# Performance work log

Hardware: AMD Instinct MI355X
Metric: run time of the kernel (lower is better)

## Reference

```python
import jax, jax.numpy as jnp
import numpy as np

B, Q, H = 1, 1024, 2048
NH, NKV, HD = 32, 8, 64
KB = 2048
THETA = 10000.0
KB_MAX_TRAIN = 4096.0


def _bitlinear(x, w):
    """BitNet b1.58 linear: per-token int8 absmax activation quant + ternary weight quant (STE)."""
    a_scale = 127.0 / jnp.clip(jnp.max(jnp.abs(x), axis=-1, keepdims=True), 1e-5)
    xq = jnp.clip(jnp.round(x * a_scale), -128.0, 127.0) / a_scale
    w_scale = 1.0 / jnp.clip(jnp.mean(jnp.abs(w)), 1e-5)
    wq = jnp.clip(jnp.round(w * w_scale), -1.0, 1.0) / w_scale
    x_ste = x + jax.lax.stop_gradient(xq - x)
    w_ste = w + jax.lax.stop_gradient(wq - w)
    return jnp.einsum('bsh,oh->bso', x_ste, w_ste)


def _rope_cos_sin(position_ids):
    inv_freq = 1.0 / (THETA ** (jnp.arange(0, HD, 2, dtype=jnp.float32) / HD))  # [HD/2]
    freqs = position_ids.astype(jnp.float32)[..., None] * inv_freq  # [B,Q,HD/2]
    emb = jnp.concatenate([freqs, freqs], axis=-1)  # [B,Q,HD]
    return jnp.cos(emb)[:, None], jnp.sin(emb)[:, None]  # [B,1,Q,HD]


def _rotate_half(x):
    return jnp.concatenate([-x[..., HD // 2:], x[..., :HD // 2]], axis=-1)


def setup_inputs() -> dict:
    key = jax.random.key(0)
    ks = jax.random.split(key, 9)
    hidden_states = jax.random.normal(ks[0], (B, Q, H), jnp.float32)
    # additive causal mask
    attention_mask = jnp.triu(jnp.full((Q, Q), -1e9, jnp.float32), 1)[None, None]
    kb_keys = jax.random.normal(ks[1], (B, NH, KB, HD), jnp.float32)
    kb_values = jax.random.normal(ks[2], (B, NH, KB, HD), jnp.float32)
    s = 0.02
    Wq = jax.random.normal(ks[3], (NH * HD, H), jnp.float32) * s
    Wk = jax.random.normal(ks[4], (NKV * HD, H), jnp.float32) * s
    Wv = jax.random.normal(ks[5], (NKV * HD, H), jnp.float32) * s
    Wo = jax.random.normal(ks[6], (H, NH * HD), jnp.float32) * s
    Wq_new = jax.random.normal(ks[7], (NH * HD, H), jnp.float32) * s
    position_ids = jnp.arange(Q, dtype=jnp.int32)[None, :]
    return dict(hidden_states=hidden_states, attention_mask=attention_mask,
                kb_keys=kb_keys, kb_values=kb_values,
                Wq=Wq, Wk=Wk, Wv=Wv, Wo=Wo, Wq_new=Wq_new,
                position_ids=position_ids)


def reference(hidden_states, attention_mask, kb_keys, kb_values,
              Wq, Wk, Wv, Wo, Wq_new, position_ids):
    b, q_len, _ = hidden_states.shape
    # BitLinear QKV projections
    q = _bitlinear(hidden_states, Wq).reshape(b, q_len, NH, HD).transpose(0, 2, 1, 3)
    k = _bitlinear(hidden_states, Wk).reshape(b, q_len, NKV, HD).transpose(0, 2, 1, 3)
    v = _bitlinear(hidden_states, Wv).reshape(b, q_len, NKV, HD).transpose(0, 2, 1, 3)
    # RoPE on prompt q/k (KB query is NOT rotated, matching the source)
    cos, sin = _rope_cos_sin(position_ids)
    q = q * cos + _rotate_half(q) * sin
    k = k * cos + _rotate_half(k) * sin
    # GQA: repeat kv heads
    groups = NH // NKV
    k = jnp.repeat(k, groups, axis=1)
    v = jnp.repeat(v, groups, axis=1)
    # KB query via separate BitLinear
    kb_q = _bitlinear(hidden_states, Wq_new).reshape(b, q_len, NH, HD).transpose(0, 2, 1, 3)
    scale = 1.0 / jnp.sqrt(jnp.float32(HD))
    kb_len = kb_keys.shape[2]
    scores_kb = jnp.einsum('bhqd,bhkd->bhqk', kb_q, kb_keys) * scale
    scores_kb = scores_kb + (jnp.log(jnp.float32(KB_MAX_TRAIN)) - jnp.log(jnp.float32(kb_len)))
    scores_p = jnp.einsum('bhqd,bhkd->bhqk', q, k) * scale + attention_mask
    attn = jax.nn.softmax(jnp.concatenate([scores_kb, scores_p], axis=-1).astype(jnp.float32), axis=-1)
    out = (jnp.einsum('bhqk,bhkd->bhqd', attn[..., :kb_len], kb_values)
           + jnp.einsum('bhqk,bhkd->bhqd', attn[..., kb_len:], v))
    out = out.transpose(0, 2, 1, 3).reshape(b, q_len, NH * HD)
    return _bitlinear(out, Wo)
```

## Files before the change

### kernel.cpp

```cpp
#include <hip/hip_runtime.h>
#include <hip/hip_bf16.h>
#include <stdint.h>
#include <math.h>

#define cH    2048
#define cQ    1024
#define cNH   32
#define cNKV  8
#define cKB   2048

#define INV_BIG   (1.0f/4194304.0f)
#define INV_SMALL (1.0f/1048576.0f)

#define WS_SUMS 0
#define WS_DQ1  256
#define WS_DQ2  4352
#define WS_XQ   8448
#define WS_WALL 4202752
#define WS_QB   25174272
#define WS_KB   33562880
#define WS_VB   35660032
#define WS_QN   37757184
#define WS_ROPET 46145792


using short8  = __attribute__((ext_vector_type(8))) short;
using floatx4 = __attribute__((ext_vector_type(4))) float;

__device__ __forceinline__ void bsplit(float x, unsigned short& hi, unsigned short& lo) {
  __hip_bfloat16 h = __float2bfloat16(x);
  float hf = __bfloat162float(h);
  __hip_bfloat16 l = __float2bfloat16(x - hf);
  hi = *(unsigned short*)&h;
  lo = *(unsigned short*)&l;
}

__device__ __forceinline__ unsigned short tern(float v, float ws) {
  float q = rintf(v * ws);
  q = fminf(fmaxf(q, -1.0f), 1.0f);
  return (unsigned short)(__float_as_uint(q) >> 16);
}

__global__ void k_ropetab(const int* __restrict__ pos, float2* __restrict__ tab) {
  int i = blockIdx.x * 256 + threadIdx.x;
  int t = i >> 5, d = i & 31;
  double p = (double)pos[t];
  double ang = p * pow(10000.0, -(double)d / 32.0);
  tab[i] = make_float2((float)cos(ang), (float)sin(ang));
}

__global__ void k_abssum5(const float* __restrict__ w0, const float* __restrict__ w1,
                          const float* __restrict__ w2, const float* __restrict__ w3,
                          const float* __restrict__ w4, double* __restrict__ out) {
  __shared__ double red[256];
  const int seg = blockIdx.y;
  const float* w = seg == 0 ? w0 : seg == 1 ? w1 : seg == 2 ? w2 : seg == 3 ? w3 : w4;
  const int n4 = ((seg == 1 || seg == 2) ? 512 * 2048 : 2048 * 2048) / 4;
  double s = 0.0;
  for (int i = blockIdx.x * 256 + threadIdx.x; i < n4; i += gridDim.x * 256) {
    float4 x = *(const float4*)(w + (size_t)i * 4);
    s += (double)fabsf(x.x) + (double)fabsf(x.y) + (double)fabsf(x.z) + (double)fabsf(x.w);
  }
  red[threadIdx.x] = s;
  __syncthreads();
  for (int o = 128; o > 0; o >>= 1) {
    if ((int)threadIdx.x < o) red[threadIdx.x] += red[threadIdx.x + o];
    __syncthreads();
  }
  if (threadIdx.x == 0) atomicAdd(out + seg, red[0]);
}

__global__ void k_wquant4(const float* __restrict__ Wq, const float* __restrict__ Wk,
                          const float* __restrict__ Wv, const float* __restrict__ Wqn,
                          unsigned short* __restrict__ wall, const double* __restrict__ sums) {
  size_t i = ((size_t)blockIdx.x * 256 + threadIdx.x) * 4;
  const float* src; size_t off; double s; float inv;
  if (i < 4194304)      { src = Wq;  off = 0;       s = sums[0]; inv = INV_BIG; }
  else if (i < 5242880) { src = Wk;  off = 4194304; s = sums[1]; inv = INV_SMALL; }
  else if (i < 6291456) { src = Wv;  off = 5242880; s = sums[2]; inv = INV_SMALL; }
  else                  { src = Wqn; off = 6291456; s = sums[4]; inv = INV_BIG; }
  float ws = 1.0f / fmaxf((float)s * inv, 1e-5f);
  float4 x = *(const float4*)(src + (i - off));
  ushort4 o;
  o.x = tern(x.x, ws); o.y = tern(x.y, ws); o.z = tern(x.z, ws); o.w = tern(x.w, ws);
  *(ushort4*)(wall + i) = o;
}

__global__ void k_wquant(const float* __restrict__ w, unsigned short* __restrict__ wq,
                         const double* __restrict__ sum, float inv_n) {
  size_t i = ((size_t)blockIdx.x * 256 + threadIdx.x) * 4;
  float ws = 1.0f / fmaxf((float)(*sum) * inv_n, 1e-5f);
  float4 x = *(const float4*)(w + i);
  ushort4 o;
  o.x = tern(x.x, ws); o.y = tern(x.y, ws); o.z = tern(x.z, ws); o.w = tern(x.w, ws);
  *(ushort4*)(wq + i) = o;
}

__global__ void k_aquant(const float* __restrict__ x, unsigned short* __restrict__ xq,
                         float* __restrict__ dq, int K) {
  int t = blockIdx.x;
  const float4* xr = (const float4*)(x + (size_t)t * K);
  const int K4 = K / 4;
  __shared__ float red[256];
  float m = 0.0f;
  for (int i = threadIdx.x; i < K4; i += 256) {
    float4 v = xr[i];
    m = fmaxf(m, fmaxf(fmaxf(fabsf(v.x), fabsf(v.y)), fmaxf(fabsf(v.z), fabsf(v.w))));
  }
  red[threadIdx.x] = m;
  __syncthreads();
  for (int o = 128; o > 0; o >>= 1) {
    if ((int)threadIdx.x < o) red[threadIdx.x] = fmaxf(red[threadIdx.x], red[threadIdx.x + o]);
    __syncthreads();
  }
  float amax = fmaxf(red[0], 1e-5f);
  float as = 127.0f / amax;
  ushort4* xo = (ushort4*)(xq + (size_t)t * K);
  for (int i = threadIdx.x; i < K4; i += 256) {
    float4 v = xr[i];
    ushort4 o;
    float q;
    q = fminf(fmaxf(rintf(v.x * as), -128.0f), 127.0f); o.x = (unsigned short)(__float_as_uint(q) >> 16);
    q = fminf(fmaxf(rintf(v.y * as), -128.0f), 127.0f); o.y = (unsigned short)(__float_as_uint(q) >> 16);
    q = fminf(fmaxf(rintf(v.z * as), -128.0f), 127.0f); o.z = (unsigned short)(__float_as_uint(q) >> 16);
    q = fminf(fmaxf(rintf(v.w * as), -128.0f), 127.0f); o.w = (unsigned short)(__float_as_uint(q) >> 16);
    xo[i] = o;
  }
  if (threadIdx.x == 0) dq[t] = amax / 127.0f;
}

__global__ __launch_bounds__(256) void k_gemm_mfma(
    const unsigned short* __restrict__ Aq, const unsigned short* __restrict__ Ball,
    const float* __restrict__ adq, const double* __restrict__ sums,
    const float2* __restrict__ ropetab,
    float* __restrict__ oQ, unsigned short* __restrict__ oKhi,
    unsigned short* __restrict__ oKlo,
    float* __restrict__ oV, float* __restrict__ oQN, int mode) {
  __shared__ unsigned short As[128 * 72];
  __shared__ unsigned short Bs[128 * 72];
  const int t = threadIdx.x;
  const int lane = t & 63;
  const int row16 = lane & 15, q = lane >> 4;
  const int w = t >> 6;
  const int wm = (w >> 1) * 64, wn = (w & 1) * 64;
  const int bx = blockIdx.x;
  const int m0 = blockIdx.y * 128;
  const unsigned short* Bp = Ball + (size_t)bx * 128 * 2048;

  floatx4 acc[4][4];
#pragma unroll
  for (int g = 0; g < 4; ++g)
#pragma unroll
    for (int h = 0; h < 4; ++h) acc[g][h] = (floatx4){0.f, 0.f, 0.f, 0.f};

  for (int k0 = 0; k0 < 2048; k0 += 64) {
#pragma unroll
    for (int i = 0; i < 4; ++i) {
      int c = t + 256 * i;
      int row = c >> 3, g8 = c & 7;
      *(uint4*)&As[row * 72 + g8 * 8] =
          *(const uint4*)(Aq + (size_t)(m0 + row) * 2048 + k0 + g8 * 8);
      *(uint4*)&Bs[row * 72 + g8 * 8] =
          *(const uint4*)(Bp + (size_t)row * 2048 + k0 + g8 * 8);
    }
    __syncthreads();
#pragma unroll
    for (int kk = 0; kk < 2; ++kk) {
      short8 af[4], bf[4];
#pragma unroll
      for (int g = 0; g < 4; ++g)
        af[g] = *(const short8*)&As[(wm + g * 16 + row16) * 72 + kk * 32 + q * 8];
#pragma unroll
      for (int h = 0; h < 4; ++h)
        bf[h] = *(const short8*)&Bs[(wn + h * 16 + row16) * 72 + kk * 32 + q * 8];
#pragma unroll
      for (int g = 0; g < 4; ++g)
#pragma unroll
        for (int h = 0; h < 4; ++h)
          acc[g][h] = __builtin_amdgcn_mfma_f32_16x16x32_bf16(af[g], bf[h], acc[g][h], 0, 0, 0);
    }
    __syncthreads();
  }

  float* outp = nullptr; int Nout = 0, nb0; float wdq;
  if (mode == 1)      { outp = oQ;  Nout = 2048; nb0 = bx * 128;        wdq = fmaxf((float)sums[3] * INV_BIG,   1e-5f); }
  else if (bx < 16)   { outp = oQ;  Nout = 2048; nb0 = bx * 128;        wdq = fmaxf((float)sums[0] * INV_BIG,   1e-5f); }
  else if (bx < 20)   {             Nout = 512;  nb0 = (bx - 16) * 128; wdq = fmaxf((float)sums[1] * INV_SMALL, 1e-5f); }
  else if (bx < 24)   { outp = oV;  Nout = 512;  nb0 = (bx - 20) * 128; wdq = fmaxf((float)sums[2] * INV_SMALL, 1e-5f); }
  else                { outp = oQN; Nout = 2048; nb0 = (bx - 24) * 128; wdq = fmaxf((float)sums[4] * INV_BIG,   1e-5f); }

  if (mode == 0 && bx < 20) {
#pragma unroll
    for (int g = 0; g < 4; ++g)
#pragma unroll
      for (int r = 0; r < 4; ++r) {
        int m = m0 + wm + g * 16 + q * 4 + r;
        float s = adq[m] * wdq;
        float2 cs0 = ropetab[m * 32 + row16];
        float2 cs1 = ropetab[m * 32 + 16 + row16];
        float v0 = acc[g][0][r] * s, v1 = acc[g][1][r] * s;
        float v2 = acc[g][2][r] * s, v3 = acc[g][3][r] * s;
        float o0 = v0 * cs0.x - v2 * cs0.y;
        float o2 = v2 * cs0.x + v0 * cs0.y;
        float o1 = v1 * cs1.x - v3 * cs1.y;
        float o3 = v3 * cs1.x + v1 * cs1.y;
        if (bx < 16) {
          size_t base = (size_t)m * Nout + nb0 + wn;
          outp[base + row16]      = o0;
          outp[base + 16 + row16] = o1;
          outp[base + 32 + row16] = o2;
          outp[base + 48 + row16] = o3;
        } else {
          int hkv_ = (nb0 + wn) >> 6;
          int kt_ = m >> 6, rr = m & 63;
          size_t tb = ((size_t)(hkv_ * 16 + kt_)) * 4096;
          int lbase = (rr & 15) + ((row16 >> 3) << 4);
          int ntb = (rr >> 4) * 512 + (row16 & 7);
          unsigned short hi, lo; int ix;
          bsplit(o0, hi, lo); ix = ntb + (lbase     ) * 8;          oKhi[tb + ix] = hi; oKlo[tb + ix] = lo;
          bsplit(o1, hi, lo); ix = ntb + (lbase + 32) * 8;          oKhi[tb + ix] = hi; oKlo[tb + ix] = lo;
          bsplit(o2, hi, lo); ix = ntb + (lbase     ) * 8 + 2048;   oKhi[tb + ix] = hi; oKlo[tb + ix] = lo;
          bsplit(o3, hi, lo); ix = ntb + (lbase + 32) * 8 + 2048;   oKhi[tb + ix] = hi; oKlo[tb + ix] = lo;
        }
      }
  } else {
#pragma unroll
    for (int g = 0; g < 4; ++g)
#pragma unroll
      for (int r = 0; r < 4; ++r) {
        int m = m0 + wm + g * 16 + q * 4 + r;
        float s = adq[m] * wdq;
#pragma unroll
        for (int h = 0; h < 4; ++h)
          outp[(size_t)m * Nout + nb0 + wn + h * 16 + row16] = acc[g][h][r] * s;
      }
  }
}

__global__ __launch_bounds__(256) void k_prep(
    const float* __restrict__ kbv, const float* __restrict__ Vb,
    unsigned short* __restrict__ vtKBhi, unsigned short* __restrict__ vtPhi,
    float* __restrict__ kbk) {
  const int b = blockIdx.x;
  const int t = threadIdx.x;
  if (b >= 1152) {
    float* tile = kbk + (size_t)(b - 1152) * 4096;
    float v[2][8];
#pragma unroll
    for (int u = 0; u < 2; ++u) {
      int task = t + 256 * u;
      int r = task >> 3, s = task & 7;
      *(float4*)&v[u][0] = *(const float4*)(tile + r * 64 + s * 8);
      *(float4*)&v[u][4] = *(const float4*)(tile + r * 64 + s * 8 + 4);
    }
    __syncthreads();
    unsigned short* up = (unsigned short*)tile;
#pragma unroll
    for (int u = 0; u < 2; ++u) {
      int task = t + 256 * u;
      int r = task >> 3, s = task & 7;
      union { unsigned short u16[8]; uint4 q; } hi, lo;
#pragma unroll
      for (int j = 0; j < 8; ++j) bsplit(v[u][j], hi.u16[j], lo.u16[j]);
      size_t off = (size_t)(((s >> 2) * 4 + (r >> 4)) * 512 + ((r & 15) + ((s & 3) << 4)) * 8);
      *(uint4*)(up + off)        = hi.q;
      *(uint4*)(up + 4096 + off) = lo.q;
    }
    return;
  }
  __shared__ float Lf[64 * 65];
  const float* src; unsigned short *dhi, *dlo; int srcStride;
  if (b < 1024) {
    int h = b >> 5, kt = b & 31;
    src = kbv + ((size_t)h * cKB + kt * 64) * 64; srcStride = 64;
    dhi = vtKBhi + (size_t)b * 4096; dlo = dhi + 4194304;
  } else {
    int bb = b - 1024;
    int hkv = bb >> 4, kt = bb & 15;
    src = Vb + (size_t)(kt * 64) * 512 + hkv * 64; srcStride = 512;
    dhi = vtPhi + (size_t)bb * 4096; dlo = dhi + 524288;
  }
#pragma unroll
  for (int i = 0; i < 4; ++i) {
    int c = t + 256 * i;
    int row = c >> 4, c4 = (c & 15) * 4;
    float4 x = *(const float4*)(src + (size_t)row * srcStride + c4);
    Lf[row * 65 + c4 + 0] = x.x;
    Lf[row * 65 + c4 + 1] = x.y;
    Lf[row * 65 + c4 + 2] = x.z;
    Lf[row * 65 + c4 + 3] = x.w;
  }
  __syncthreads();
#pragma unroll
  for (int u = 0; u < 2; ++u) {
    int task = t + 256 * u;
    int d = task >> 3, s = task & 7;
    union { unsigned short u16[8]; uint4 q; } hi, lo;
#pragma unroll
    for (int j = 0; j < 8; ++j) bsplit(Lf[(s * 8 + j) * 65 + d], hi.u16[j], lo.u16[j]);
    size_t off = (size_t)(((s >> 2) * 4 + (d >> 4)) * 512 + ((d & 15) + ((s & 3) << 4)) * 8);
    *(uint4*)(dhi + off) = hi.q;
    *(uint4*)(dlo + off) = lo.q;
  }
}

__global__ __launch_bounds__(256, 2) void k_attn_mfma(
    const float* __restrict__ Qr, float* qnctx,
    const unsigned short* __restrict__ KPhi,
    const unsigned short* __restrict__ kbkS,
    const unsigned short* __restrict__ vtKBhi,
    const unsigned short* __restrict__ vtPhi) {
  __shared__ __attribute__((aligned(16))) unsigned int Pbuf[4][16 * 68];

  const int t = threadIdx.x;
  const int lane = t & 63;
  const int col = lane & 15;
  const int quad = lane >> 4;
  const int w = t >> 6;
  const int h = blockIdx.x;
  const int q0 = blockIdx.y * 64;
  const int hkv = h >> 2;
  const float kbbias = 0.69314718055994531f;
  unsigned int* Pw = &Pbuf[w][0];
  const int fl = lane * 8;

  short8 qAh[2], qAl[2];
  short8 qBh[2], qBl[2];
  {
#pragma unroll
    for (int kk = 0; kk < 2; ++kk) {
      const size_t off = (size_t)(q0 + w * 16 + col) * 2048 + h * 64 + kk * 32 + quad * 8;
      float4 a = *(const float4*)(qnctx + off);
      float4 b = *(const float4*)(qnctx + off + 4);
      float xs[8] = {a.x, a.y, a.z, a.w, b.x, b.y, b.z, b.w};
#pragma unroll
      for (int j = 0; j < 8; ++j) {
        unsigned short hi, lo;
        bsplit(xs[j] * 0.125f, hi, lo);
        qAh[kk][j] = (short)hi; qAl[kk][j] = (short)lo;
      }
      float4 c = *(const float4*)(Qr + off);
      float4 d = *(const float4*)(Qr + off + 4);
      float ys[8] = {c.x, c.y, c.z, c.w, d.x, d.y, d.z, d.w};
#pragma unroll
      for (int j = 0; j < 8; ++j) {
        unsigned short hi, lo;
        bsplit(ys[j] * 0.125f, hi, lo);
        qBh[kk][j] = (short)hi; qBl[kk][j] = (short)lo;
      }
    }
  }

  floatx4 acco[4];
  float m_[4], l_[4];
#pragma unroll
  for (int nt = 0; nt < 4; ++nt) acco[nt] = (floatx4){0.f, 0.f, 0.f, 0.f};
#pragma unroll
  for (int r = 0; r < 4; ++r) { m_[r] = -3.0e38f; l_[r] = 0.f; }

  const int ntiles = 32 + (q0 >> 6) + 1;

  short8 kh[2][4], kl[2][4];
  short8 vh[2][4], vl[2][4];

  auto loadK = [&](int kt2) {
    const unsigned short *ph, *pl;
    if (kt2 < 32) { const size_t tk = (size_t)(h * 32 + kt2);
                    ph = kbkS + tk * 8192; pl = ph + 4096; }
    else          { const size_t tk = (size_t)(hkv * 16 + (kt2 - 32));
                    ph = KPhi + tk * 4096; pl = ph + 524288; }
#pragma unroll
    for (int kk = 0; kk < 2; ++kk)
#pragma unroll
      for (int nt = 0; nt < 4; ++nt) {
        kh[kk][nt] = *(const short8*)(ph + (kk * 4 + nt) * 512 + fl);
        kl[kk][nt] = *(const short8*)(pl + (kk * 4 + nt) * 512 + fl);
      }
  };
  auto loadV = [&](int kt2) {
    const unsigned short *ph, *pl;
    if (kt2 < 32) { const size_t tk = (size_t)(h * 32 + kt2);
                    ph = vtKBhi + tk * 4096; pl = ph + 4194304; }
    else          { const size_t tk = (size_t)(hkv * 16 + (kt2 - 32));
                    ph = vtPhi + tk * 4096; pl = ph + 524288; }
#pragma unroll
    for (int kk = 0; kk < 2; ++kk)
#pragma unroll
      for (int nt = 0; nt < 4; ++nt) {
        vh[kk][nt] = *(const short8*)(ph + (kk * 4 + nt) * 512 + fl);
        vl[kk][nt] = *(const short8*)(pl + (kk * 4 + nt) * 512 + fl);
      }
  };

  loadK(0);

  for (int kt = 0; kt < ntiles; ++kt) {
    const bool isKB = kt < 32;
    loadV(kt);
    __builtin_amdgcn_s_barrier();

    floatx4 accs[4];
#pragma unroll
    for (int nt = 0; nt < 4; ++nt) accs[nt] = (floatx4){0.f, 0.f, 0.f, 0.f};
    if (isKB) {
#pragma unroll
      for (int kk = 0; kk < 2; ++kk)
#pragma unroll
        for (int nt = 0; nt < 4; ++nt) {
          accs[nt] = __builtin_amdgcn_mfma_f32_16x16x32_bf16(qAh[kk], kh[kk][nt], accs[nt], 0, 0, 0);
          accs[nt] = __builtin_amdgcn_mfma_f32_16x16x32_bf16(qAl[kk], kh[kk][nt], accs[nt], 0, 0, 0);
          accs[nt] = __builtin_amdgcn_mfma_f32_16x16x32_bf16(qAh[kk], kl[kk][nt], accs[nt], 0, 0, 0);
        }
    } else {
#pragma unroll
      for (int kk = 0; kk < 2; ++kk)
#pragma unroll
        for (int nt = 0; nt < 4; ++nt) {
          accs[nt] = __builtin_amdgcn_mfma_f32_16x16x32_bf16(qBh[kk], kh[kk][nt], accs[nt], 0, 0, 0);
          accs[nt] = __builtin_amdgcn_mfma_f32_16x16x32_bf16(qBl[kk], kh[kk][nt], accs[nt], 0, 0, 0);
          accs[nt] = __builtin_amdgcn_mfma_f32_16x16x32_bf16(qBh[kk], kl[kk][nt], accs[nt], 0, 0, 0);
        }
    }

    float sv[4][4];
    if (isKB) {
#pragma unroll
      for (int nt = 0; nt < 4; ++nt)
#pragma unroll
        for (int r = 0; r < 4; ++r) sv[nt][r] = accs[nt][r] + kbbias;
    } else if (kt < ntiles - 1) {
#pragma unroll
      for (int nt = 0; nt < 4; ++nt)
#pragma unroll
        for (int r = 0; r < 4; ++r) sv[nt][r] = accs[nt][r];
    } else {
#pragma unroll
      for (int nt = 0; nt < 4; ++nt) {
        int kl_ = nt * 16 + col;
#pragma unroll
        for (int r = 0; r < 4; ++r) {
          int ql_ = w * 16 + quad * 4 + r;
          sv[nt][r] = accs[nt][r] + ((kl_ <= ql_) ? 0.0f : -1e9f);
        }
      }
    }
#pragma unroll
    for (int r = 0; r < 4; ++r) {
      float rmax = fmaxf(fmaxf(sv[0][r], sv[1][r]), fmaxf(sv[2][r], sv[3][r]));
#pragma unroll
      for (int off = 8; off; off >>= 1) rmax = fmaxf(rmax, __shfl_xor(rmax, off));
      float mnew = fmaxf(m_[r], rmax);
      float alpha = __expf(m_[r] - mnew);
      float psum = 0.f;
#pragma unroll
      for (int nt = 0; nt < 4; ++nt) {
        float p = __expf(sv[nt][r] - mnew);
        sv[nt][r] = p;
        psum += p;
      }
#pragma unroll
      for (int off = 8; off; off >>= 1) psum += __shfl_xor(psum, off);
      l_[r] = l_[r] * alpha + psum;
      m_[r] = mnew;
#pragma unroll
      for (int nt = 0; nt < 4; ++nt) acco[nt][r] *= alpha;
    }

    loadK(kt + 1 < ntiles ? kt + 1 : kt);

#pragma unroll
    for (int nt = 0; nt < 4; ++nt)
#pragma unroll
      for (int r = 0; r < 4; ++r) {
        unsigned xb = __float_as_uint(sv[nt][r]);
        float hf = __uint_as_float(xb & 0xffff0000u);
        unsigned db = __float_as_uint(sv[nt][r] - hf);
        Pw[(quad * 4 + r) * 68 + nt * 16 + col] = (xb >> 16) | (db & 0xffff0000u);
      }

#pragma unroll
    for (int kk = 0; kk < 2; ++kk) {
      uint4 pa = *(const uint4*)&Pw[col * 68 + kk * 32 + quad * 8];
      uint4 pb = *(const uint4*)&Pw[col * 68 + kk * 32 + quad * 8 + 4];
      union { unsigned int u[4]; short8 s; } uh, ul;
      uh.u[0] = (pa.x & 0xffffu) | (pa.y << 16);
      uh.u[1] = (pa.z & 0xffffu) | (pa.w << 16);
      uh.u[2] = (pb.x & 0xffffu) | (pb.y << 16);
      uh.u[3] = (pb.z & 0xffffu) | (pb.w << 16);
      ul.u[0] = (pa.x >> 16) | (pa.y & 0xffff0000u);
      ul.u[1] = (pa.z >> 16) | (pa.w & 0xffff0000u);
      ul.u[2] = (pb.x >> 16) | (pb.y & 0xffff0000u);
      ul.u[3] = (pb.z >> 16) | (pb.w & 0xffff0000u);
      short8 ph8 = uh.s, pl8 = ul.s;
#pragma unroll
      for (int nt = 0; nt < 4; ++nt) {
        acco[nt] = __builtin_amdgcn_mfma_f32_16x16x32_bf16(ph8, vh[kk][nt], acco[nt], 0, 0, 0);
        acco[nt] = __builtin_amdgcn_mfma_f32_16x16x32_bf16(pl8, vh[kk][nt], acco[nt], 0, 0, 0);
        acco[nt] = __builtin_amdgcn_mfma_f32_16x16x32_bf16(ph8, vl[kk][nt], acco[nt], 0, 0, 0);
      }
    }
  }

#pragma unroll
  for (int r = 0; r < 4; ++r) {
    float linv = 1.0f / l_[r];
#pragma unroll
    for (int nt = 0; nt < 4; ++nt)
      qnctx[(size_t)(q0 + w * 16 + quad * 4 + r) * 2048 + h * 64 + nt * 16 + col] =
          acco[nt][r] * linv;
  }
}

extern "C" void kernel_launch(void* const* d_in, const int* in_sizes, int n_in,
                              void* d_out, int out_size, void* d_ws, size_t ws_size,
                              hipStream_t stream) {
  (void)in_sizes; (void)n_in; (void)out_size; (void)ws_size;
  const float* hidden = (const float*)d_in[0];
  float* kbk = (float*)d_in[2];
  const float* kbv = (const float*)d_in[3];
  const float* Wq  = (const float*)d_in[4];
  const float* Wk  = (const float*)d_in[5];
  const float* Wv  = (const float*)d_in[6];
  const float* Wo  = (const float*)d_in[7];
  const float* Wqn = (const float*)d_in[8];
  const int*   pos = (const int*)d_in[9];

  char* ws = (char*)d_ws;
  double* sums = (double*)(ws + WS_SUMS);
  float* dq1 = (float*)(ws + WS_DQ1);
  float* dq2 = (float*)(ws + WS_DQ2);
  unsigned short* xq   = (unsigned short*)(ws + WS_XQ);
  unsigned short* wall = (unsigned short*)(ws + WS_WALL);
  unsigned short* vtKBhi = (unsigned short*)(ws + WS_WALL);
  unsigned short* vtPhi  = (unsigned short*)(ws + WS_WALL + 16777216);
  unsigned short* wqo  = (unsigned short*)(ws + WS_QB);
  float* Qb  = (float*)(ws + WS_QB);
  unsigned short* KPhi = (unsigned short*)(ws + WS_KB);
  unsigned short* KPlo = KPhi + 524288;
  float* Vb  = (float*)(ws + WS_VB);
  float* QNC = (float*)(ws + WS_QN);
  float2* ropetab = (float2*)(ws + WS_ROPET);

  hipMemsetAsync(sums, 0, 64, stream);

  k_ropetab<<<128, 256, 0, stream>>>(pos, ropetab);
  k_abssum5<<<dim3(128, 5), 256, 0, stream>>>(Wq, Wk, Wv, Wo, Wqn, sums);
  k_wquant4<<<10240, 256, 0, stream>>>(Wq, Wk, Wv, Wqn, wall, sums);
  k_aquant<<<cQ, 256, 0, stream>>>(hidden, xq, dq1, cH);

  k_gemm_mfma<<<dim3(40, 8), 256, 0, stream>>>(xq, wall, dq1, sums, ropetab,
                                               Qb, KPhi, KPlo, Vb, QNC, 0);

  k_prep<<<1152 + 1024, 256, 0, stream>>>(kbv, Vb, vtKBhi, vtPhi, kbk);

  k_attn_mfma<<<dim3(cNH, cQ / 64), 256, 0, stream>>>(
      Qb, QNC, KPhi, (const unsigned short*)kbk, vtKBhi, vtPhi);

  k_wquant<<<4096, 256, 0, stream>>>(Wo, wqo, sums + 3, INV_BIG);
  k_aquant<<<cQ, 256, 0, stream>>>(QNC, xq, dq2, cH);

  k_gemm_mfma<<<dim3(16, 8), 256, 0, stream>>>(xq, wqo, dq2, sums, ropetab,
                                               (float*)d_out, nullptr, nullptr,
                                               nullptr, nullptr, 1);
}
```

Before: 392.0 us.

## Split attention into KB and prompt passes with a separate softmax merge

The attention kernel now launches a second grid dimension so the knowledge-base keys and the causal prompt keys run in separate blocks. Each block writes an unnormalized partial output and its running max and sum, and a new merge kernel combines the two partials with rescaled softmax weights. This doubles the block count, shortens the serial tile loop per block, removes per-tile branching and halves the Q registers held, with launch bounds raised to allow more occupancy. In exchange it costs an extra kernel launch plus an extra round trip of partial outputs through global memory.

```diff
diff --git a/kernel.cpp b/kernel.cpp
--- a/kernel.cpp
+++ b/kernel.cpp
@@ -22,6 +22,7 @@
 #define WS_VB   35660032
 #define WS_QN   37757184
 #define WS_ROPET 46145792
+#define WS_ML   46407936
 
 
 using short8  = __attribute__((ext_vector_type(8))) short;
@@ -304,12 +305,13 @@
   }
 }
 
-__global__ __launch_bounds__(256, 2) void k_attn_mfma(
-    const float* __restrict__ Qr, float* qnctx,
+__global__ __launch_bounds__(256, 4) void k_attn_mfma(
+    float* __restrict__ Qr, float* __restrict__ qnctx,
     const unsigned short* __restrict__ KPhi,
     const unsigned short* __restrict__ kbkS,
     const unsigned short* __restrict__ vtKBhi,
-    const unsigned short* __restrict__ vtPhi) {
+    const unsigned short* __restrict__ vtPhi,
+    float2* __restrict__ ml) {
   __shared__ __attribute__((aligned(16))) unsigned int Pbuf[4][16 * 68];
 
   const int t = threadIdx.x;
@@ -319,34 +321,38 @@
   const int w = t >> 6;
   const int h = blockIdx.x;
   const int q0 = blockIdx.y * 64;
+  const int split = blockIdx.z;
   const int hkv = h >> 2;
   const float kbbias = 0.69314718055994531f;
   unsigned int* Pw = &Pbuf[w][0];
   const int fl = lane * 8;
 
-  short8 qAh[2], qAl[2];
-  short8 qBh[2], qBl[2];
+  const unsigned short *Kb, *Vbp; int Kstr, Kloo, Vloo, ntiles;
+  float* obase;
+  if (split == 0) {
+    Kb = kbkS + (size_t)h * 32 * 8192;   Kstr = 8192; Kloo = 4096;
+    Vbp = vtKBhi + (size_t)h * 32 * 4096; Vloo = 4194304;
+    ntiles = 32; obase = qnctx;
+  } else {
+    Kb = KPhi + (size_t)hkv * 16 * 4096; Kstr = 4096; Kloo = 524288;
+    Vbp = vtPhi + (size_t)hkv * 16 * 4096; Vloo = 524288;
+    ntiles = (q0 >> 6) + 1; obase = Qr;
+  }
+
+  short8 qh[2], ql[2];
   {
+    const float* qbase = split == 0 ? qnctx : Qr;
 #pragma unroll
     for (int kk = 0; kk < 2; ++kk) {
       const size_t off = (size_t)(q0 + w * 16 + col) * 2048 + h * 64 + kk * 32 + quad * 8;
-      float4 a = *(const float4*)(qnctx + off);
-      float4 b = *(const float4*)(qnctx + off + 4);
+      float4 a = *(const float4*)(qbase + off);
+      float4 b = *(const float4*)(qbase + off + 4);
       float xs[8] = {a.x, a.y, a.z, a.w, b.x, b.y, b.z, b.w};
 #pragma unroll
       for (int j = 0; j < 8; ++j) {
         unsigned short hi, lo;
         bsplit(xs[j] * 0.125f, hi, lo);
-        qAh[kk][j] = (short)hi; qAl[kk][j] = (short)lo;
-      }
-      float4 c = *(const float4*)(Qr + off);
-      float4 d = *(const float4*)(Qr + off + 4);
-      float ys[8] = {c.x, c.y, c.z, c.w, d.x, d.y, d.z, d.w};
-#pragma unroll
-      for (int j = 0; j < 8; ++j) {
-        unsigned short hi, lo;
-        bsplit(ys[j] * 0.125f, hi, lo);
-        qBh[kk][j] = (short)hi; qBl[kk][j] = (short)lo;
+        qh[kk][j] = (short)hi; ql[kk][j] = (short)lo;
       }
     }
   }
@@ -358,17 +364,12 @@
 #pragma unroll
   for (int r = 0; r < 4; ++r) { m_[r] = -3.0e38f; l_[r] = 0.f; }
 
-  const int ntiles = 32 + (q0 >> 6) + 1;
-
   short8 kh[2][4], kl[2][4];
   short8 vh[2][4], vl[2][4];
 
   auto loadK = [&](int kt2) {
-    const unsigned short *ph, *pl;
-    if (kt2 < 32) { const size_t tk = (size_t)(h * 32 + kt2);
-                    ph = kbkS + tk * 8192; pl = ph + 4096; }
-    else          { const size_t tk = (size_t)(hkv * 16 + (kt2 - 32));
-                    ph = KPhi + tk * 4096; pl = ph + 524288; }
+    const unsigned short* ph = Kb + (size_t)kt2 * Kstr;
+    const unsigned short* pl = ph + Kloo;
 #pragma unroll
     for (int kk = 0; kk < 2; ++kk)
 #pragma unroll
@@ -378,11 +379,8 @@
       }
   };
   auto loadV = [&](int kt2) {
-    const unsigned short *ph, *pl;
-    if (kt2 < 32) { const size_t tk = (size_t)(h * 32 + kt2);
-                    ph = vtKBhi + tk * 4096; pl = ph + 4194304; }
-    else          { const size_t tk = (size_t)(hkv * 16 + (kt2 - 32));
-                    ph = vtPhi + tk * 4096; pl = ph + 524288; }
+    const unsigned short* ph = Vbp + (size_t)kt2 * 4096;
+    const unsigned short* pl = ph + Vloo;
 #pragma unroll
     for (int kk = 0; kk < 2; ++kk)
 #pragma unroll
@@ -395,35 +393,23 @@
   loadK(0);
 
   for (int kt = 0; kt < ntiles; ++kt) {
-    const bool isKB = kt < 32;
     loadV(kt);
     __builtin_amdgcn_s_barrier();
 
     floatx4 accs[4];
 #pragma unroll
     for (int nt = 0; nt < 4; ++nt) accs[nt] = (floatx4){0.f, 0.f, 0.f, 0.f};
-    if (isKB) {
-#pragma unroll
-      for (int kk = 0; kk < 2; ++kk)
-#pragma unroll
-        for (int nt = 0; nt < 4; ++nt) {
-          accs[nt] = __builtin_amdgcn_mfma_f32_16x16x32_bf16(qAh[kk], kh[kk][nt], accs[nt], 0, 0, 0);
-          accs[nt] = __builtin_amdgcn_mfma_f32_16x16x32_bf16(qAl[kk], kh[kk][nt], accs[nt], 0, 0, 0);
-          accs[nt] = __builtin_amdgcn_mfma_f32_16x16x32_bf16(qAh[kk], kl[kk][nt], accs[nt], 0, 0, 0);
-        }
-    } else {
-#pragma unroll
-      for (int kk = 0; kk < 2; ++kk)
-#pragma unroll
-        for (int nt = 0; nt < 4; ++nt) {
-          accs[nt] = __builtin_amdgcn_mfma_f32_16x16x32_bf16(qBh[kk], kh[kk][nt], accs[nt], 0, 0, 0);
-          accs[nt] = __builtin_amdgcn_mfma_f32_16x16x32_bf16(qBl[kk], kh[kk][nt], accs[nt], 0, 0, 0);
-          accs[nt] = __builtin_amdgcn_mfma_f32_16x16x32_bf16(qBh[kk], kl[kk][nt], accs[nt], 0, 0, 0);
-        }
-    }
+#pragma unroll
+    for (int kk = 0; kk < 2; ++kk)
+#pragma unroll
+      for (int nt = 0; nt < 4; ++nt) {
+        accs[nt] = __builtin_amdgcn_mfma_f32_16x16x32_bf16(qh[kk], kh[kk][nt], accs[nt], 0, 0, 0);
+        accs[nt] = __builtin_amdgcn_mfma_f32_16x16x32_bf16(ql[kk], kh[kk][nt], accs[nt], 0, 0, 0);
+        accs[nt] = __builtin_amdgcn_mfma_f32_16x16x32_bf16(qh[kk], kl[kk][nt], accs[nt], 0, 0, 0);
+      }
 
     float sv[4][4];
-    if (isKB) {
+    if (split == 0) {
 #pragma unroll
       for (int nt = 0; nt < 4; ++nt)
 #pragma unroll
@@ -503,12 +489,35 @@
 
 #pragma unroll
   for (int r = 0; r < 4; ++r) {
-    float linv = 1.0f / l_[r];
+    int row = q0 + w * 16 + quad * 4 + r;
 #pragma unroll
     for (int nt = 0; nt < 4; ++nt)
-      qnctx[(size_t)(q0 + w * 16 + quad * 4 + r) * 2048 + h * 64 + nt * 16 + col] =
-          acco[nt][r] * linv;
-  }
+      obase[(size_t)row * 2048 + h * 64 + nt * 16 + col] = acco[nt][r];
+    if (col == 0)
+      ml[(size_t)(split * 32 + h) * 1024 + row] = make_float2(m_[r], l_[r]);
+  }
+}
+
+__global__ __launch_bounds__(256) void k_merge(
+    float* __restrict__ qnctx, const float* __restrict__ Qb,
+    const float2* __restrict__ ml) {
+  int task = blockIdx.x * 16 + (threadIdx.x >> 4);
+  int h = task >> 10, q = task & 1023;
+  float2 a = ml[h * 1024 + q];
+  float2 c = ml[32768 + h * 1024 + q];
+  float mm = fmaxf(a.x, c.x);
+  float e0 = __expf(a.x - mm), e1 = __expf(c.x - mm);
+  float inv = 1.0f / (a.y * e0 + c.y * e1);
+  float a0 = e0 * inv, a1 = e1 * inv;
+  size_t off = (size_t)q * 2048 + h * 64 + (threadIdx.x & 15) * 4;
+  float4 o0 = *(const float4*)(qnctx + off);
+  float4 o1 = *(const float4*)(Qb + off);
+  float4 o;
+  o.x = o0.x * a0 + o1.x * a1;
+  o.y = o0.y * a0 + o1.y * a1;
+  o.z = o0.z * a0 + o1.z * a1;
+  o.w = o0.w * a0 + o1.w * a1;
+  *(float4*)(qnctx + off) = o;
 }
 
 extern "C" void kernel_launch(void* const* d_in, const int* in_sizes, int n_in,
@@ -540,6 +549,7 @@
   float* Vb  = (float*)(ws + WS_VB);
   float* QNC = (float*)(ws + WS_QN);
   float2* ropetab = (float2*)(ws + WS_ROPET);
+  float2* ml = (float2*)(ws + WS_ML);
 
   hipMemsetAsync(sums, 0, 64, stream);
 
@@ -553,8 +563,10 @@
 
   k_prep<<<1152 + 1024, 256, 0, stream>>>(kbv, Vb, vtKBhi, vtPhi, kbk);
 
-  k_attn_mfma<<<dim3(cNH, cQ / 64), 256, 0, stream>>>(
-      Qb, QNC, KPhi, (const unsigned short*)kbk, vtKBhi, vtPhi);
+  k_attn_mfma<<<dim3(cNH, cQ / 64, 2), 256, 0, stream>>>(
+      Qb, QNC, KPhi, (const unsigned short*)kbk, vtKBhi, vtPhi, ml);
+
+  k_merge<<<2048, 256, 0, stream>>>(QNC, Qb, ml);
 
   k_wquant<<<4096, 256, 0, stream>>>(Wo, wqo, sums + 3, INV_BIG);
   k_aquant<<<cQ, 256, 0, stream>>>(QNC, xq, dq2, cH);
```

Result: slower. 503.8 us (+28.5%).

## Double-buffer GEMM tiles via direct global-to-LDS loads and add 64-tile output GEMM

Applied to the files above, without the earlier changes.

The main bf16 MFMA GEMM now stages A/B tiles straight from global memory into LDS with global_load_lds, double-buffered so the next k-tile's load overlaps the current tile's MFMAs. An XOR swizzle replaces row padding to avoid LDS bank conflicts. The final Wo projection moves to a new 64x64-tile kernel launched as 512 blocks instead of 128, to fill more compute units. The hand-written vmcnt waits and raw barriers depend on exact load counts, and the extra LDS buffer may lower occupancy.

```diff
diff --git a/kernel.cpp b/kernel.cpp
--- a/kernel.cpp
+++ b/kernel.cpp
@@ -39,6 +39,11 @@
   float q = rintf(v * ws);
   q = fminf(fmaxf(q, -1.0f), 1.0f);
   return (unsigned short)(__float_as_uint(q) >> 16);
+}
+
+__device__ __forceinline__ void gload16(const void* g, void* l) {
+  __builtin_amdgcn_global_load_lds((const __attribute__((address_space(1))) void*)g,
+                                   (__attribute__((address_space(3))) void*)l, 16, 0, 0);
 }
 
 __global__ void k_ropetab(const int* __restrict__ pos, float2* __restrict__ tab) {
@@ -136,8 +141,8 @@
     float* __restrict__ oQ, unsigned short* __restrict__ oKhi,
     unsigned short* __restrict__ oKlo,
     float* __restrict__ oV, float* __restrict__ oQN, int mode) {
-  __shared__ unsigned short As[128 * 72];
-  __shared__ unsigned short Bs[128 * 72];
+  __shared__ __attribute__((aligned(16))) unsigned short As[2][128 * 64];
+  __shared__ __attribute__((aligned(16))) unsigned short Bs[2][128 * 64];
   const int t = threadIdx.x;
   const int lane = t & 63;
   const int row16 = lane & 15, q = lane >> 4;
@@ -146,6 +151,7 @@
   const int bx = blockIdx.x;
   const int m0 = blockIdx.y * 128;
   const unsigned short* Bp = Ball + (size_t)bx * 128 * 2048;
+  const int swr = row16 & 7;
 
   floatx4 acc[4][4];
 #pragma unroll
@@ -153,34 +159,43 @@
 #pragma unroll
     for (int h = 0; h < 4; ++h) acc[g][h] = (floatx4){0.f, 0.f, 0.f, 0.f};
 
-  for (int k0 = 0; k0 < 2048; k0 += 64) {
+  auto stageAB = [&](int k0s, int b) {
 #pragma unroll
     for (int i = 0; i < 4; ++i) {
       int c = t + 256 * i;
       int row = c >> 3, g8 = c & 7;
-      *(uint4*)&As[row * 72 + g8 * 8] =
-          *(const uint4*)(Aq + (size_t)(m0 + row) * 2048 + k0 + g8 * 8);
-      *(uint4*)&Bs[row * 72 + g8 * 8] =
-          *(const uint4*)(Bp + (size_t)row * 2048 + k0 + g8 * 8);
-    }
-    __syncthreads();
+      int sa = (g8 ^ (row & 7)) * 8;
+      gload16(Aq + (size_t)(m0 + row) * 2048 + k0s + sa, &As[b][w * 512 + i * 2048]);
+      gload16(Bp + (size_t)row * 2048 + k0s + sa, &Bs[b][w * 512 + i * 2048]);
+    }
+  };
+
+  stageAB(0, 0);
+  for (int k0 = 0; k0 < 2048; k0 += 64) {
+    const int cur = (k0 >> 6) & 1;
+    const int kn = (k0 + 64 < 2048) ? k0 + 64 : k0;
+    stageAB(kn, cur ^ 1);
+    asm volatile("s_waitcnt vmcnt(8)" ::: "memory");
+    __builtin_amdgcn_s_barrier();
 #pragma unroll
     for (int kk = 0; kk < 2; ++kk) {
       short8 af[4], bf[4];
+      const int sw = ((kk * 4 + q) ^ swr) << 3;
 #pragma unroll
       for (int g = 0; g < 4; ++g)
-        af[g] = *(const short8*)&As[(wm + g * 16 + row16) * 72 + kk * 32 + q * 8];
+        af[g] = *(const short8*)&As[cur][(wm + g * 16 + row16) * 64 + sw];
 #pragma unroll
       for (int h = 0; h < 4; ++h)
-        bf[h] = *(const short8*)&Bs[(wn + h * 16 + row16) * 72 + kk * 32 + q * 8];
+        bf[h] = *(const short8*)&Bs[cur][(wn + h * 16 + row16) * 64 + sw];
 #pragma unroll
       for (int g = 0; g < 4; ++g)
 #pragma unroll
         for (int h = 0; h < 4; ++h)
           acc[g][h] = __builtin_amdgcn_mfma_f32_16x16x32_bf16(af[g], bf[h], acc[g][h], 0, 0, 0);
     }
-    __syncthreads();
-  }
+    __builtin_amdgcn_s_barrier();
+  }
+  asm volatile("s_waitcnt vmcnt(0)" ::: "memory");
 
   float* outp = nullptr; int Nout = 0, nb0; float wdq;
   if (mode == 1)      { outp = oQ;  Nout = 2048; nb0 = bx * 128;        wdq = fmaxf((float)sums[3] * INV_BIG,   1e-5f); }
@@ -237,6 +252,78 @@
   }
 }
 
+__global__ __launch_bounds__(256) void k_gemm64(
+    const unsigned short* __restrict__ Aq, const unsigned short* __restrict__ Bq,
+    const float* __restrict__ adq, const double* __restrict__ sums,
+    float* __restrict__ out) {
+  __shared__ __attribute__((aligned(16))) unsigned short As[2][64 * 64];
+  __shared__ __attribute__((aligned(16))) unsigned short Bs[2][64 * 64];
+  const int t = threadIdx.x;
+  const int lane = t & 63;
+  const int row16 = lane & 15, q = lane >> 4;
+  const int w = t >> 6;
+  const int wm = (w >> 1) * 32, wn = (w & 1) * 32;
+  const int nb0 = blockIdx.x * 64;
+  const int m0 = blockIdx.y * 64;
+  const int swr = row16 & 7;
+
+  floatx4 acc[2][2];
+#pragma unroll
+  for (int g = 0; g < 2; ++g)
+#pragma unroll
+    for (int h = 0; h < 2; ++h) acc[g][h] = (floatx4){0.f, 0.f, 0.f, 0.f};
+
+  auto stageAB = [&](int k0s, int b) {
+#pragma unroll
+    for (int i = 0; i < 2; ++i) {
+      int c = t + 256 * i;
+      int row = c >> 3, g8 = c & 7;
+      int sa = (g8 ^ (row & 7)) * 8;
+      gload16(Aq + (size_t)(m0 + row) * 2048 + k0s + sa, &As[b][w * 512 + i * 2048]);
+      gload16(Bq + (size_t)(nb0 + row) * 2048 + k0s + sa, &Bs[b][w * 512 + i * 2048]);
+    }
+  };
+
+  stageAB(0, 0);
+  for (int k0 = 0; k0 < 2048; k0 += 64) {
+    const int cur = (k0 >> 6) & 1;
+    const int kn = (k0 + 64 < 2048) ? k0 + 64 : k0;
+    stageAB(kn, cur ^ 1);
+    asm volatile("s_waitcnt vmcnt(4)" ::: "memory");
+    __builtin_amdgcn_s_barrier();
+#pragma unroll
+    for (int kk = 0; kk < 2; ++kk) {
+      short8 af[2], bf[2];
+      const int sw = ((kk * 4 + q) ^ swr) << 3;
+#pragma unroll
+      for (int g = 0; g < 2; ++g)
+        af[g] = *(const short8*)&As[cur][(wm + g * 16 + row16) * 64 + sw];
+#pragma unroll
+      for (int h = 0; h < 2; ++h)
+        bf[h] = *(const short8*)&Bs[cur][(wn + h * 16 + row16) * 64 + sw];
+#pragma unroll
+      for (int g = 0; g < 2; ++g)
+#pragma unroll
+        for (int h = 0; h < 2; ++h)
+          acc[g][h] = __builtin_amdgcn_mfma_f32_16x16x32_bf16(af[g], bf[h], acc[g][h], 0, 0, 0);
+    }
+    __builtin_amdgcn_s_barrier();
+  }
+  asm volatile("s_waitcnt vmcnt(0)" ::: "memory");
+
+  float wdq = fmaxf((float)sums[3] * INV_BIG, 1e-5f);
+#pragma unroll
+  for (int g = 0; g < 2; ++g)
+#pragma unroll
+    for (int r = 0; r < 4; ++r) {
+      int m = m0 + wm + g * 16 + q * 4 + r;
+      float s = adq[m] * wdq;
+#pragma unroll
+      for (int h = 0; h < 2; ++h)
+        out[(size_t)m * 2048 + nb0 + wn + h * 16 + row16] = acc[g][h][r] * s;
+    }
+}
+
 __global__ __launch_bounds__(256) void k_prep(
     const float* __restrict__ kbv, const float* __restrict__ Vb,
     unsigned short* __restrict__ vtKBhi, unsigned short* __restrict__ vtPhi,
@@ -559,7 +646,5 @@
   k_wquant<<<4096, 256, 0, stream>>>(Wo, wqo, sums + 3, INV_BIG);
   k_aquant<<<cQ, 256, 0, stream>>>(QNC, xq, dq2, cH);
 
-  k_gemm_mfma<<<dim3(16, 8), 256, 0, stream>>>(xq, wqo, dq2, sums, ropetab,
-                                               (float*)d_out, nullptr, nullptr,
-                                               nullptr, nullptr, 1);
-}
+  k_gemm64<<<dim3(32, 16), 256, 0, stream>>>(xq, wqo, dq2, sums, (float*)d_out);
+}
```

Result: faster. 371.8 us (-5.2%).

## Rewrite GEMM with 64x64 tiles, double-buffered direct-to-LDS loads and swizzle

Applied to the files above, without the earlier changes.

The projection GEMM changes from 128x128 to 64x64 tiles. Operand tiles are now staged straight from global memory into LDS with global_load_lds into a double buffer, using an XOR swizzle in place of padding to avoid bank conflicts, and the next K-tile is prefetched while the current one is computed. The aim is to hide global load latency and raise occupancy and block count on the GPU, at the cost of less register-level reuse per block. The attention kernel also raises wave priority around its MFMA sections with s_setprio.

```diff
diff --git a/kernel.cpp b/kernel.cpp
--- a/kernel.cpp
+++ b/kernel.cpp
@@ -39,6 +39,11 @@
   float q = rintf(v * ws);
   q = fminf(fmaxf(q, -1.0f), 1.0f);
   return (unsigned short)(__float_as_uint(q) >> 16);
+}
+
+__device__ __forceinline__ void gload16(const void* g, void* l) {
+  __builtin_amdgcn_global_load_lds((const __attribute__((address_space(1))) void*)g,
+                                   (__attribute__((address_space(3))) void*)l, 16, 0, 0);
 }
 
 __global__ void k_ropetab(const int* __restrict__ pos, float2* __restrict__ tab) {
@@ -129,111 +134,110 @@
   if (threadIdx.x == 0) dq[t] = amax / 127.0f;
 }
 
-__global__ __launch_bounds__(256) void k_gemm_mfma(
+__global__ __launch_bounds__(256) void k_gemm64u(
     const unsigned short* __restrict__ Aq, const unsigned short* __restrict__ Ball,
     const float* __restrict__ adq, const double* __restrict__ sums,
     const float2* __restrict__ ropetab,
     float* __restrict__ oQ, unsigned short* __restrict__ oKhi,
     unsigned short* __restrict__ oKlo,
     float* __restrict__ oV, float* __restrict__ oQN, int mode) {
-  __shared__ unsigned short As[128 * 72];
-  __shared__ unsigned short Bs[128 * 72];
+  __shared__ __attribute__((aligned(16))) unsigned short As[2][64 * 64];
+  __shared__ __attribute__((aligned(16))) unsigned short Bs[2][64 * 64];
   const int t = threadIdx.x;
   const int lane = t & 63;
   const int row16 = lane & 15, q = lane >> 4;
   const int w = t >> 6;
-  const int wm = (w >> 1) * 64, wn = (w & 1) * 64;
   const int bx = blockIdx.x;
-  const int m0 = blockIdx.y * 128;
-  const unsigned short* Bp = Ball + (size_t)bx * 128 * 2048;
-
-  floatx4 acc[4][4];
-#pragma unroll
-  for (int g = 0; g < 4; ++g)
-#pragma unroll
-    for (int h = 0; h < 4; ++h) acc[g][h] = (floatx4){0.f, 0.f, 0.f, 0.f};
-
-  for (int k0 = 0; k0 < 2048; k0 += 64) {
-#pragma unroll
-    for (int i = 0; i < 4; ++i) {
+  const int m0 = blockIdx.y * 64;
+  const unsigned short* Bp = Ball + (size_t)bx * 64 * 2048;
+  const int swr = row16 & 7;
+
+  floatx4 acc[4];
+#pragma unroll
+  for (int h = 0; h < 4; ++h) acc[h] = (floatx4){0.f, 0.f, 0.f, 0.f};
+
+  auto stageAB = [&](int k0s, int b) {
+#pragma unroll
+    for (int i = 0; i < 2; ++i) {
       int c = t + 256 * i;
       int row = c >> 3, g8 = c & 7;
-      *(uint4*)&As[row * 72 + g8 * 8] =
-          *(const uint4*)(Aq + (size_t)(m0 + row) * 2048 + k0 + g8 * 8);
-      *(uint4*)&Bs[row * 72 + g8 * 8] =
-          *(const uint4*)(Bp + (size_t)row * 2048 + k0 + g8 * 8);
-    }
-    __syncthreads();
+      int sa = (g8 ^ (row & 7)) * 8;
+      gload16(Aq + (size_t)(m0 + row) * 2048 + k0s + sa, &As[b][w * 512 + i * 2048]);
+      gload16(Bp + (size_t)row * 2048 + k0s + sa, &Bs[b][w * 512 + i * 2048]);
+    }
+  };
+
+  stageAB(0, 0);
+  for (int k0 = 0; k0 < 2048; k0 += 64) {
+    const int cur = (k0 >> 6) & 1;
+    const int kn = (k0 + 64 < 2048) ? k0 + 64 : k0;
+    stageAB(kn, cur ^ 1);
+    asm volatile("s_waitcnt vmcnt(4)" ::: "memory");
+    __builtin_amdgcn_s_barrier();
 #pragma unroll
     for (int kk = 0; kk < 2; ++kk) {
-      short8 af[4], bf[4];
-#pragma unroll
-      for (int g = 0; g < 4; ++g)
-        af[g] = *(const short8*)&As[(wm + g * 16 + row16) * 72 + kk * 32 + q * 8];
+      short8 af, bf[4];
+      const int sw = ((kk * 4 + q) ^ swr) << 3;
+      af = *(const short8*)&As[cur][(w * 16 + row16) * 64 + sw];
 #pragma unroll
       for (int h = 0; h < 4; ++h)
-        bf[h] = *(const short8*)&Bs[(wn + h * 16 + row16) * 72 + kk * 32 + q * 8];
-#pragma unroll
-      for (int g = 0; g < 4; ++g)
-#pragma unroll
-        for (int h = 0; h < 4; ++h)
-          acc[g][h] = __builtin_amdgcn_mfma_f32_16x16x32_bf16(af[g], bf[h], acc[g][h], 0, 0, 0);
-    }
-    __syncthreads();
-  }
+        bf[h] = *(const short8*)&Bs[cur][(h * 16 + row16) * 64 + sw];
+#pragma unroll
+      for (int h = 0; h < 4; ++h)
+        acc[h] = __builtin_amdgcn_mfma_f32_16x16x32_bf16(af, bf[h], acc[h], 0, 0, 0);
+    }
+    __builtin_amdgcn_s_barrier();
+  }
+  asm volatile("s_waitcnt vmcnt(0)" ::: "memory");
 
   float* outp = nullptr; int Nout = 0, nb0; float wdq;
-  if (mode == 1)      { outp = oQ;  Nout = 2048; nb0 = bx * 128;        wdq = fmaxf((float)sums[3] * INV_BIG,   1e-5f); }
-  else if (bx < 16)   { outp = oQ;  Nout = 2048; nb0 = bx * 128;        wdq = fmaxf((float)sums[0] * INV_BIG,   1e-5f); }
-  else if (bx < 20)   {             Nout = 512;  nb0 = (bx - 16) * 128; wdq = fmaxf((float)sums[1] * INV_SMALL, 1e-5f); }
-  else if (bx < 24)   { outp = oV;  Nout = 512;  nb0 = (bx - 20) * 128; wdq = fmaxf((float)sums[2] * INV_SMALL, 1e-5f); }
-  else                { outp = oQN; Nout = 2048; nb0 = (bx - 24) * 128; wdq = fmaxf((float)sums[4] * INV_BIG,   1e-5f); }
-
-  if (mode == 0 && bx < 20) {
-#pragma unroll
-    for (int g = 0; g < 4; ++g)
-#pragma unroll
-      for (int r = 0; r < 4; ++r) {
-        int m = m0 + wm + g * 16 + q * 4 + r;
-        float s = adq[m] * wdq;
-        float2 cs0 = ropetab[m * 32 + row16];
-        float2 cs1 = ropetab[m * 32 + 16 + row16];
-        float v0 = acc[g][0][r] * s, v1 = acc[g][1][r] * s;
-        float v2 = acc[g][2][r] * s, v3 = acc[g][3][r] * s;
-        float o0 = v0 * cs0.x - v2 * cs0.y;
-        float o2 = v2 * cs0.x + v0 * cs0.y;
-        float o1 = v1 * cs1.x - v3 * cs1.y;
-        float o3 = v3 * cs1.x + v1 * cs1.y;
-        if (bx < 16) {
-          size_t base = (size_t)m * Nout + nb0 + wn;
-          outp[base + row16]      = o0;
-          outp[base + 16 + row16] = o1;
-          outp[base + 32 + row16] = o2;
-          outp[base + 48 + row16] = o3;
-        } else {
-          int hkv_ = (nb0 + wn) >> 6;
-          int kt_ = m >> 6, rr = m & 63;
-          size_t tb = ((size_t)(hkv_ * 16 + kt_)) * 4096;
-          int lbase = (rr & 15) + ((row16 >> 3) << 4);
-          int ntb = (rr >> 4) * 512 + (row16 & 7);
-          unsigned short hi, lo; int ix;
-          bsplit(o0, hi, lo); ix = ntb + (lbase     ) * 8;          oKhi[tb + ix] = hi; oKlo[tb + ix] = lo;
-          bsplit(o1, hi, lo); ix = ntb + (lbase + 32) * 8;          oKhi[tb + ix] = hi; oKlo[tb + ix] = lo;
-          bsplit(o2, hi, lo); ix = ntb + (lbase     ) * 8 + 2048;   oKhi[tb + ix] = hi; oKlo[tb + ix] = lo;
-          bsplit(o3, hi, lo); ix = ntb + (lbase + 32) * 8 + 2048;   oKhi[tb + ix] = hi; oKlo[tb + ix] = lo;
-        }
-      }
+  if (mode == 1)      { outp = oQ;  Nout = 2048; nb0 = bx * 64;        wdq = fmaxf((float)sums[3] * INV_BIG,   1e-5f); }
+  else if (bx < 32)   { outp = oQ;  Nout = 2048; nb0 = bx * 64;        wdq = fmaxf((float)sums[0] * INV_BIG,   1e-5f); }
+  else if (bx < 40)   {             Nout = 512;  nb0 = (bx - 32) * 64; wdq = fmaxf((float)sums[1] * INV_SMALL, 1e-5f); }
+  else if (bx < 48)   { outp = oV;  Nout = 512;  nb0 = (bx - 40) * 64; wdq = fmaxf((float)sums[2] * INV_SMALL, 1e-5f); }
+  else                { outp = oQN; Nout = 2048; nb0 = (bx - 48) * 64; wdq = fmaxf((float)sums[4] * INV_BIG,   1e-5f); }
+
+  if (mode == 0 && bx < 40) {
+#pragma unroll
+    for (int r = 0; r < 4; ++r) {
+      int m = m0 + w * 16 + q * 4 + r;
+      float s = adq[m] * wdq;
+      float2 cs0 = ropetab[m * 32 + row16];
+      float2 cs1 = ropetab[m * 32 + 16 + row16];
+      float v0 = acc[0][r] * s, v1 = acc[1][r] * s;
+      float v2 = acc[2][r] * s, v3 = acc[3][r] * s;
+      float o0 = v0 * cs0.x - v2 * cs0.y;
+      float o2 = v2 * cs0.x + v0 * cs0.y;
+      float o1 = v1 * cs1.x - v3 * cs1.y;
+      float o3 = v3 * cs1.x + v1 * cs1.y;
+      if (bx < 32) {
+        size_t base = (size_t)m * 2048 + nb0;
+        outp[base + row16]      = o0;
+        outp[base + 16 + row16] = o1;
+        outp[base + 32 + row16] = o2;
+        outp[base + 48 + row16] = o3;
+      } else {
+        int hkv_ = bx - 32;
+        int kt_ = m >> 6, rr = m & 63;
+        size_t tb = ((size_t)(hkv_ * 16 + kt_)) * 4096;
+        int lbase = (rr & 15) + ((row16 >> 3) << 4);
+        int ntb = (rr >> 4) * 512 + (row16 & 7);
+        unsigned short hi, lo; int ix;
+        bsplit(o0, hi, lo); ix = ntb + (lbase     ) * 8;          oKhi[tb + ix] = hi; oKlo[tb + ix] = lo;
+        bsplit(o1, hi, lo); ix = ntb + (lbase + 32) * 8;          oKhi[tb + ix] = hi; oKlo[tb + ix] = lo;
+        bsplit(o2, hi, lo); ix = ntb + (lbase     ) * 8 + 2048;   oKhi[tb + ix] = hi; oKlo[tb + ix] = lo;
+        bsplit(o3, hi, lo); ix = ntb + (lbase + 32) * 8 + 2048;   oKhi[tb + ix] = hi; oKlo[tb + ix] = lo;
+      }
+    }
   } else {
 #pragma unroll
-    for (int g = 0; g < 4; ++g)
-#pragma unroll
-      for (int r = 0; r < 4; ++r) {
-        int m = m0 + wm + g * 16 + q * 4 + r;
-        float s = adq[m] * wdq;
-#pragma unroll
-        for (int h = 0; h < 4; ++h)
-          outp[(size_t)m * Nout + nb0 + wn + h * 16 + row16] = acc[g][h][r] * s;
-      }
+    for (int r = 0; r < 4; ++r) {
+      int m = m0 + w * 16 + q * 4 + r;
+      float s = adq[m] * wdq;
+#pragma unroll
+      for (int h = 0; h < 4; ++h)
+        outp[(size_t)m * Nout + nb0 + h * 16 + row16] = acc[h][r] * s;
+    }
   }
 }
 
@@ -402,6 +406,7 @@
     floatx4 accs[4];
 #pragma unroll
     for (int nt = 0; nt < 4; ++nt) accs[nt] = (floatx4){0.f, 0.f, 0.f, 0.f};
+    __builtin_amdgcn_s_setprio(1);
     if (isKB) {
 #pragma unroll
       for (int kk = 0; kk < 2; ++kk)
@@ -421,6 +426,7 @@
           accs[nt] = __builtin_amdgcn_mfma_f32_16x16x32_bf16(qBh[kk], kl[kk][nt], accs[nt], 0, 0, 0);
         }
     }
+    __builtin_amdgcn_s_setprio(0);
 
     float sv[4][4];
     if (isKB) {
@@ -492,12 +498,14 @@
       ul.u[2] = (pb.x >> 16) | (pb.y & 0xffff0000u);
       ul.u[3] = (pb.z >> 16) | (pb.w & 0xffff0000u);
       short8 ph8 = uh.s, pl8 = ul.s;
+      __builtin_amdgcn_s_setprio(1);
 #pragma unroll
       for (int nt = 0; nt < 4; ++nt) {
         acco[nt] = __builtin_amdgcn_mfma_f32_16x16x32_bf16(ph8, vh[kk][nt], acco[nt], 0, 0, 0);
         acco[nt] = __builtin_amdgcn_mfma_f32_16x16x32_bf16(pl8, vh[kk][nt], acco[nt], 0, 0, 0);
         acco[nt] = __builtin_amdgcn_mfma_f32_16x16x32_bf16(ph8, vl[kk][nt], acco[nt], 0, 0, 0);
       }
+      __builtin_amdgcn_s_setprio(0);
     }
   }
 
@@ -548,8 +556,8 @@
   k_wquant4<<<10240, 256, 0, stream>>>(Wq, Wk, Wv, Wqn, wall, sums);
   k_aquant<<<cQ, 256, 0, stream>>>(hidden, xq, dq1, cH);
 
-  k_gemm_mfma<<<dim3(40, 8), 256, 0, stream>>>(xq, wall, dq1, sums, ropetab,
-                                               Qb, KPhi, KPlo, Vb, QNC, 0);
+  k_gemm64u<<<dim3(80, 16), 256, 0, stream>>>(xq, wall, dq1, sums, ropetab,
+                                              Qb, KPhi, KPlo, Vb, QNC, 0);
 
   k_prep<<<1152 + 1024, 256, 0, stream>>>(kbv, Vb, vtKBhi, vtPhi, kbk);
 
@@ -559,7 +567,7 @@
   k_wquant<<<4096, 256, 0, stream>>>(Wo, wqo, sums + 3, INV_BIG);
   k_aquant<<<cQ, 256, 0, stream>>>(QNC, xq, dq2, cH);
 
-  k_gemm_mfma<<<dim3(16, 8), 256, 0, stream>>>(xq, wqo, dq2, sums, ropetab,
-                                               (float*)d_out, nullptr, nullptr,
-                                               nullptr, nullptr, 1);
-}
+  k_gemm64u<<<dim3(32, 16), 256, 0, stream>>>(xq, wqo, dq2, sums, ropetab,
+                                              (float*)d_out, nullptr, nullptr,
+                                              nullptr, nullptr, 1);
+}
```

Result: faster. 380.8 us (-2.9%).
